# Performance work log

Hardware: AMD Instinct MI355X
Metric: run time of the kernel (lower is better)

## Reference

```python
import jax, jax.numpy as jnp
import numpy as np

LAYER_START = 4
WS = 2  # context_window_size
EPS = 1e-8


def _alpha_for_k(tf, idx):
    # tf: [L, D] per-token layer features; idx: static window row indices (last entry is k)
    Wm = tf[idx]                       # [w, D]
    w = Wm.shape[0]
    _, R = jnp.linalg.qr(Wm.T)         # reduced QR of [D, w] -> R: [w, w]
    r = R[:, -1]
    sub = R[:-1, :-1]
    coln = jnp.linalg.norm(sub, axis=0)
    align = jnp.mean(sub / coln, axis=1) @ R[:-1, -1] / jnp.linalg.norm(r[:-1])
    align = 1.0 / (align * w * 2)
    nov = jnp.abs(r[-1]) / jnp.linalg.norm(r)
    return align, nov


def _unify_token(tf):
    # tf: [L, D] -> pooled [D]
    L = tf.shape[0]
    aligns, novs = [], []
    for k in range(L):  # loop over small fixed layer count (structurally distinct windows)
        # NOTE: original torch code token_feature[k-ws:k] yields an EMPTY slice for k < ws
        left = list(range(k - WS, k)) if k >= WS else []
        right = list(range(k + 1, min(k + WS + 1, L)))
        idx = np.array(left + right + [k], dtype=np.int32)
        a, n = _alpha_for_k(tf, idx)
        aligns.append(a)
        novs.append(n)
    aa = jnp.stack(aligns)
    nv = jnp.stack(novs)
    aa = aa / aa.sum()
    nv = nv / nv.sum()
    alpha = aa + nv
    alpha = alpha / alpha.sum()
    return tf.T @ alpha


def _token_var(tf):
    # tf: [L, D] -> variance (unbiased) of subdiagonal of cosine-sim map
    w = jnp.linalg.norm(tf, axis=1, keepdims=True)
    sim = (tf @ tf.T) / jnp.clip(w * w.T, EPS)
    return jnp.var(jnp.diagonal(sim, -1), ddof=1)


def reference(all_hidden_states, attention_mask):
    # all_hidden_states: [B, num_layers, S, D]; attention_mask: [B, S] (all sentences equal length)
    T = int(np.asarray(attention_mask).sum(axis=1)[0]) - 1  # unmask_num = sum(mask) - 1
    sf = all_hidden_states[:, LAYER_START:, :T, :]          # [B, L, T, D]
    per_tok = jax.vmap(jax.vmap(_unify_token, in_axes=1))(sf)  # [B, T, D]

    def per_sentence(s, ose):
        v = jax.vmap(_token_var, in_axes=1)(s)  # [T]
        v = v / v.sum()
        return ose.T @ v                        # [D]

    return jax.vmap(per_sentence)(sf, per_tok)  # [B, D]


def setup_inputs():
    key = jax.random.key(0)
    all_hidden_states = jax.random.normal(key, (8, 12, 512, 768), dtype=jnp.float32)
    attention_mask = jnp.ones((8, 512), dtype=jnp.int32)
    return {"all_hidden_states": all_hidden_states, "attention_mask": attention_mask}
```

## Files before the change

kernel.cpp:

```cpp
#include <hip/hip_runtime.h>
#include <math.h>

#define NLAYER_TOT 12
#define LAYER0 4
#define SMAX 512
#define DIM 768

__global__ void k_init(const int* __restrict__ mask, int* __restrict__ wsT,
                       float* __restrict__ out) {
    __shared__ int red[512];
    int tid = threadIdx.x;
    red[tid] = mask[tid];
    __syncthreads();
    for (int s = 256; s >= 1; s >>= 1) {
        if (tid < s) red[tid] += red[tid + s];
        __syncthreads();
    }
    if (tid == 0) wsT[0] = red[0] - 1;
    for (int i = tid; i < 8 * DIM; i += 512) out[i] = 0.0f;
}

__global__ __launch_bounds__(64) void k_gram(const float* __restrict__ in,
                                             const int* __restrict__ wsT,
                                             float* __restrict__ Gout) {
    int T = wsT[0];
    int t = blockIdx.x;
    int b = blockIdx.y;
    if (t >= T) return;
    int lane = threadIdx.x;
    const float* base = in + ((size_t)(b * NLAYER_TOT + LAYER0) * SMAX + t) * DIM;
    float acc[36];
#pragma unroll
    for (int p = 0; p < 36; ++p) acc[p] = 0.0f;
#pragma unroll
    for (int it = 0; it < 3; ++it) {
        int d = it * 256 + lane * 4;
        float4 x[8];
#pragma unroll
        for (int k = 0; k < 8; ++k)
            x[k] = *(const float4*)(base + (size_t)k * SMAX * DIM + d);
        int p = 0;
#pragma unroll
        for (int i = 0; i < 8; ++i)
#pragma unroll
            for (int j = i; j < 8; ++j) {
                acc[p] += x[i].x * x[j].x + x[i].y * x[j].y + x[i].z * x[j].z + x[i].w * x[j].w;
                ++p;
            }
    }
    float* gdst = Gout + ((size_t)b * SMAX + t) * 36;
#pragma unroll
    for (int p = 0; p < 36; ++p) {
        float v = acc[p];
#pragma unroll
        for (int off = 32; off >= 1; off >>= 1) v += __shfl_xor(v, off, 64);
        if (lane == 0) gdst[p] = v;
    }
}

template <int W>
__device__ inline void alpha_nov(const float* __restrict__ Gf, const int* __restrict__ idx,
                                 float& align_o, float& nov_o) {
    float Gs[W][W];
#pragma unroll
    for (int i = 0; i < W; ++i)
#pragma unroll
        for (int j = i; j < W; ++j) {
            float v = Gf[idx[i] * 8 + idx[j]];
            Gs[i][j] = v;
            Gs[j][i] = v;
        }
    float R[W][W];
#pragma unroll
    for (int j = 0; j < W; ++j) {
#pragma unroll
        for (int i = 0; i <= j; ++i) {
            float s = Gs[i][j];
#pragma unroll
            for (int q = 0; q < i; ++q) s -= R[q][i] * R[q][j];
            R[i][j] = (i == j) ? sqrtf(s) : (s / R[i][i]);
        }
    }
    float ic[W - 1];
#pragma unroll
    for (int j = 0; j < W - 1; ++j) ic[j] = 1.0f / sqrtf(Gs[j][j]);
    float m[W - 1];
#pragma unroll
    for (int i = 0; i < W - 1; ++i) {
        float s = 0.0f;
#pragma unroll
        for (int j = i; j < W - 1; ++j) s += R[i][j] * ic[j];
        m[i] = s * (1.0f / (float)(W - 1));
    }
    float num = 0.0f, n1 = 0.0f;
#pragma unroll
    for (int i = 0; i < W - 1; ++i) {
        num += m[i] * R[i][W - 1];
        n1 += R[i][W - 1] * R[i][W - 1];
    }
    float align_raw = num / sqrtf(n1);
    align_o = 1.0f / (align_raw * (float)W * 2.0f);
    nov_o = fabsf(R[W - 1][W - 1]) / sqrtf(Gs[W - 1][W - 1]);
}

__global__ __launch_bounds__(64) void k_alpha(const int* __restrict__ wsT,
                                              const float* __restrict__ Gin,
                                              float* __restrict__ alpha,
                                              float* __restrict__ vraw) {
    int T = wsT[0];
    int id = blockIdx.x * 64 + threadIdx.x;
    int b = id >> 9;
    int t = id & 511;
    if (b >= 8 || t >= T) return;
    float Gf[64];
    const float* gsrc = Gin + ((size_t)b * SMAX + t) * 36;
    {
        int p = 0;
#pragma unroll
        for (int i = 0; i < 8; ++i)
#pragma unroll
            for (int j = i; j < 8; ++j) {
                float v = gsrc[p++];
                Gf[i * 8 + j] = v;
                Gf[j * 8 + i] = v;
            }
    }
    static constexpr int IDX0[5] = {1, 2, 0, 0, 0};
    static constexpr int IDX1[5] = {2, 3, 1, 0, 0};
    static constexpr int IDX2[5] = {0, 1, 3, 4, 2};
    static constexpr int IDX3[5] = {1, 2, 4, 5, 3};
    static constexpr int IDX4[5] = {2, 3, 5, 6, 4};
    static constexpr int IDX5[5] = {3, 4, 6, 7, 5};
    static constexpr int IDX6[5] = {4, 5, 7, 6, 0};
    static constexpr int IDX7[5] = {5, 6, 7, 0, 0};
    float a[8], n[8];
    alpha_nov<3>(Gf, IDX0, a[0], n[0]);
    alpha_nov<3>(Gf, IDX1, a[1], n[1]);
    alpha_nov<5>(Gf, IDX2, a[2], n[2]);
    alpha_nov<5>(Gf, IDX3, a[3], n[3]);
    alpha_nov<5>(Gf, IDX4, a[4], n[4]);
    alpha_nov<5>(Gf, IDX5, a[5], n[5]);
    alpha_nov<4>(Gf, IDX6, a[6], n[6]);
    alpha_nov<3>(Gf, IDX7, a[7], n[7]);
    float sa = 0.0f, sn = 0.0f;
#pragma unroll
    for (int k = 0; k < 8; ++k) { sa += a[k]; sn += n[k]; }
    float isa = 1.0f / sa, isn = 1.0f / sn;
    float al[8], ss = 0.0f;
#pragma unroll
    for (int k = 0; k < 8; ++k) { al[k] = a[k] * isa + n[k] * isn; ss += al[k]; }
    float iss = 1.0f / ss;
    float* adst = alpha + ((size_t)b * SMAX + t) * 8;
#pragma unroll
    for (int k = 0; k < 8; ++k) adst[k] = al[k] * iss;
    float c[7], mu = 0.0f;
#pragma unroll
    for (int i = 0; i < 7; ++i) {
        float denom = sqrtf(Gf[i * 8 + i]) * sqrtf(Gf[(i + 1) * 8 + (i + 1)]);
        denom = denom > 1e-8f ? denom : 1e-8f;
        c[i] = Gf[(i + 1) * 8 + i] / denom;
        mu += c[i];
    }
    mu *= (1.0f / 7.0f);
    float var = 0.0f;
#pragma unroll
    for (int i = 0; i < 7; ++i) var += (c[i] - mu) * (c[i] - mu);
    vraw[(size_t)b * SMAX + t] = var * (1.0f / 6.0f);
}

__global__ void k_weights(const int* __restrict__ wsT, const float* __restrict__ alpha,
                          const float* __restrict__ vraw, float* __restrict__ W) {
    int T = wsT[0];
    int b = blockIdx.x;
    int tid = threadIdx.x;
    __shared__ float red[256];
    float s = 0.0f;
    for (int t = tid; t < T; t += 256) s += vraw[(size_t)b * SMAX + t];
    red[tid] = s;
    __syncthreads();
    for (int k = 128; k >= 1; k >>= 1) {
        if (tid < k) red[tid] += red[tid + k];
        __syncthreads();
    }
    float inv = 1.0f / red[0];
    for (int t = tid; t < T; t += 256) {
        float v = vraw[(size_t)b * SMAX + t] * inv;
#pragma unroll
        for (int k = 0; k < 8; ++k)
            W[((size_t)b * SMAX + t) * 8 + k] = alpha[((size_t)b * SMAX + t) * 8 + k] * v;
    }
}

__global__ void k_out(const float* __restrict__ in, const int* __restrict__ wsT,
                      const float* __restrict__ W, float* __restrict__ out) {
    int T = wsT[0];
    int tseg = blockIdx.x;
    int dchunk = blockIdx.y;
    int b = blockIdx.z;
    int d = dchunk * 256 + threadIdx.x;
    int t0 = tseg * 16;
    int t1 = min(t0 + 16, T);
    if (t0 >= t1) return;
    const float* base = in + ((size_t)(b * NLAYER_TOT + LAYER0) * SMAX) * DIM + d;
    const float* wb = W + (size_t)b * SMAX * 8;
    float acc = 0.0f;
    for (int t = t0; t < t1; ++t) {
#pragma unroll
        for (int k = 0; k < 8; ++k)
            acc += wb[t * 8 + k] * base[((size_t)k * SMAX + t) * DIM];
    }
    atomicAdd(&out[b * DIM + d], acc);
}

extern "C" void kernel_launch(void* const* d_in, const int* in_sizes, int n_in,
                              void* d_out, int out_size, void* d_ws, size_t ws_size,
                              hipStream_t stream) {
    const float* hs = (const float*)d_in[0];
    const int* mask = (const int*)d_in[1];
    float* out = (float*)d_out;
    char* ws = (char*)d_ws;
    int* wsT = (int*)ws;
    float* G = (float*)(ws + 256);
    float* alpha = (float*)(ws + 256 + (size_t)8 * 512 * 36 * 4);
    float* vraw = (float*)(ws + 256 + (size_t)(8 * 512 * 36 + 8 * 512 * 8) * 4);
    float* W = (float*)(ws + 256 + (size_t)(8 * 512 * 36 + 8 * 512 * 8 + 8 * 512) * 4);

    k_init<<<1, 512, 0, stream>>>(mask, wsT, out);
    k_gram<<<dim3(SMAX - 1, 8), 64, 0, stream>>>(hs, wsT, G);
    k_alpha<<<64, 64, 0, stream>>>(wsT, G, alpha, vraw);
    k_weights<<<8, 256, 0, stream>>>(wsT, alpha, vraw, W);
    k_out<<<dim3(32, 3, 8), 256, 0, stream>>>(hs, wsT, W, out);
}
```

Baseline: 249.6 us.

## Fuse gram, alpha, weights and output into one kernel with deferred normalization

Merges the gram, alpha/variance, weight and output-accumulation kernels into a single per-token kernel. The gram reduction is broadcast to all lanes, every lane redundantly computes the alpha weights, and the token's own rows are re-read (likely from cache) to accumulate a weighted sum into the output with atomics. Normalization by the variance sum is deferred to a small scale kernel, using an atomically accumulated per-sentence sum. This removes the intermediate global buffers and two launches, and swaps divides and sqrts for fast rcp/rsq intrinsics, at the cost of heavy float atomics on 768 output addresses per sentence and slightly lower precision.

```diff
diff --git a/kernel.cpp b/kernel.cpp
--- a/kernel.cpp
+++ b/kernel.cpp
@@ -6,8 +6,16 @@
 #define SMAX 512
 #define DIM 768
 
+__host__ __device__ constexpr int gp(int i, int j) {
+    return (i <= j) ? (i * 8 - i * (i - 1) / 2 + (j - i))
+                    : (j * 8 - j * (j - 1) / 2 + (i - j));
+}
+
+__device__ inline float frcp(float x) { return __builtin_amdgcn_rcpf(x); }
+__device__ inline float frsq(float x) { return __builtin_amdgcn_rsqf(x); }
+
 __global__ void k_init(const int* __restrict__ mask, int* __restrict__ wsT,
-                       float* __restrict__ out) {
+                       float* __restrict__ out, float* __restrict__ vsum) {
     __shared__ int red[512];
     int tid = threadIdx.x;
     red[tid] = mask[tid];
@@ -18,17 +26,66 @@
     }
     if (tid == 0) wsT[0] = red[0] - 1;
     for (int i = tid; i < 8 * DIM; i += 512) out[i] = 0.0f;
+    if (tid < 8) vsum[tid] = 0.0f;
 }
 
-__global__ __launch_bounds__(64) void k_gram(const float* __restrict__ in,
-                                             const int* __restrict__ wsT,
-                                             float* __restrict__ Gout) {
+template <int W>
+__device__ inline void alpha_nov(const float (&A)[36], const int (&idx)[5],
+                                 float& align_o, float& nov_o) {
+    float Gs[W][W];
+#pragma unroll
+    for (int i = 0; i < W; ++i)
+#pragma unroll
+        for (int j = i; j < W; ++j) {
+            float v = A[gp(idx[i], idx[j])];
+            Gs[i][j] = v;
+            Gs[j][i] = v;
+        }
+    float R[W][W];
+#pragma unroll
+    for (int j = 0; j < W; ++j) {
+#pragma unroll
+        for (int i = 0; i <= j; ++i) {
+            float s = Gs[i][j];
+#pragma unroll
+            for (int q = 0; q < i; ++q) s -= R[q][i] * R[q][j];
+            if (i == j) R[i][j] = s * frsq(s);
+            else        R[i][j] = s * frcp(R[i][i]);
+        }
+    }
+    float ic[W - 1];
+#pragma unroll
+    for (int j = 0; j < W - 1; ++j) ic[j] = frsq(Gs[j][j]);
+    float m[W - 1];
+#pragma unroll
+    for (int i = 0; i < W - 1; ++i) {
+        float s = 0.0f;
+#pragma unroll
+        for (int j = i; j < W - 1; ++j) s += R[i][j] * ic[j];
+        m[i] = s * (1.0f / (float)(W - 1));
+    }
+    float num = 0.0f, n1 = 0.0f;
+#pragma unroll
+    for (int i = 0; i < W - 1; ++i) {
+        num += m[i] * R[i][W - 1];
+        n1 += R[i][W - 1] * R[i][W - 1];
+    }
+    float align_raw = num * frsq(n1);
+    align_o = frcp(align_raw * (float)W * 2.0f);
+    nov_o = fabsf(R[W - 1][W - 1]) * frsq(Gs[W - 1][W - 1]);
+}
+
+__global__ __launch_bounds__(64) void k_fused(const float* __restrict__ in,
+                                              const int* __restrict__ wsT,
+                                              float* __restrict__ out,
+                                              float* __restrict__ vsum) {
     int T = wsT[0];
     int t = blockIdx.x;
     int b = blockIdx.y;
     if (t >= T) return;
     int lane = threadIdx.x;
     const float* base = in + ((size_t)(b * NLAYER_TOT + LAYER0) * SMAX + t) * DIM;
+
     float acc[36];
 #pragma unroll
     for (int p = 0; p < 36; ++p) acc[p] = 0.0f;
@@ -48,83 +105,12 @@
                 ++p;
             }
     }
-    float* gdst = Gout + ((size_t)b * SMAX + t) * 36;
 #pragma unroll
     for (int p = 0; p < 36; ++p) {
-        float v = acc[p];
 #pragma unroll
-        for (int off = 32; off >= 1; off >>= 1) v += __shfl_xor(v, off, 64);
-        if (lane == 0) gdst[p] = v;
+        for (int off = 32; off >= 1; off >>= 1) acc[p] += __shfl_xor(acc[p], off, 64);
     }
-}
 
-template <int W>
-__device__ inline void alpha_nov(const float* __restrict__ Gf, const int* __restrict__ idx,
-                                 float& align_o, float& nov_o) {
-    float Gs[W][W];
-#pragma unroll
-    for (int i = 0; i < W; ++i)
-#pragma unroll
-        for (int j = i; j < W; ++j) {
-            float v = Gf[idx[i] * 8 + idx[j]];
-            Gs[i][j] = v;
-            Gs[j][i] = v;
-        }
-    float R[W][W];
-#pragma unroll
-    for (int j = 0; j < W; ++j) {
-#pragma unroll
-        for (int i = 0; i <= j; ++i) {
-            float s = Gs[i][j];
-#pragma unroll
-            for (int q = 0; q < i; ++q) s -= R[q][i] * R[q][j];
-            R[i][j] = (i == j) ? sqrtf(s) : (s / R[i][i]);
-        }
-    }
-    float ic[W - 1];
-#pragma unroll
-    for (int j = 0; j < W - 1; ++j) ic[j] = 1.0f / sqrtf(Gs[j][j]);
-    float m[W - 1];
-#pragma unroll
-    for (int i = 0; i < W - 1; ++i) {
-        float s = 0.0f;
-#pragma unroll
-        for (int j = i; j < W - 1; ++j) s += R[i][j] * ic[j];
-        m[i] = s * (1.0f / (float)(W - 1));
-    }
-    float num = 0.0f, n1 = 0.0f;
-#pragma unroll
-    for (int i = 0; i < W - 1; ++i) {
-        num += m[i] * R[i][W - 1];
-        n1 += R[i][W - 1] * R[i][W - 1];
-    }
-    float align_raw = num / sqrtf(n1);
-    align_o = 1.0f / (align_raw * (float)W * 2.0f);
-    nov_o = fabsf(R[W - 1][W - 1]) / sqrtf(Gs[W - 1][W - 1]);
-}
-
-__global__ __launch_bounds__(64) void k_alpha(const int* __restrict__ wsT,
-                                              const float* __restrict__ Gin,
-                                              float* __restrict__ alpha,
-                                              float* __restrict__ vraw) {
-    int T = wsT[0];
-    int id = blockIdx.x * 64 + threadIdx.x;
-    int b = id >> 9;
-    int t = id & 511;
-    if (b >= 8 || t >= T) return;
-    float Gf[64];
-    const float* gsrc = Gin + ((size_t)b * SMAX + t) * 36;
-    {
-        int p = 0;
-#pragma unroll
-        for (int i = 0; i < 8; ++i)
-#pragma unroll
-            for (int j = i; j < 8; ++j) {
-                float v = gsrc[p++];
-                Gf[i * 8 + j] = v;
-                Gf[j * 8 + i] = v;
-            }
-    }
     static constexpr int IDX0[5] = {1, 2, 0, 0, 0};
     static constexpr int IDX1[5] = {2, 3, 1, 0, 0};
     static constexpr int IDX2[5] = {0, 1, 3, 4, 2};
@@ -134,82 +120,64 @@
     static constexpr int IDX6[5] = {4, 5, 7, 6, 0};
     static constexpr int IDX7[5] = {5, 6, 7, 0, 0};
     float a[8], n[8];
-    alpha_nov<3>(Gf, IDX0, a[0], n[0]);
-    alpha_nov<3>(Gf, IDX1, a[1], n[1]);
-    alpha_nov<5>(Gf, IDX2, a[2], n[2]);
-    alpha_nov<5>(Gf, IDX3, a[3], n[3]);
-    alpha_nov<5>(Gf, IDX4, a[4], n[4]);
-    alpha_nov<5>(Gf, IDX5, a[5], n[5]);
-    alpha_nov<4>(Gf, IDX6, a[6], n[6]);
-    alpha_nov<3>(Gf, IDX7, a[7], n[7]);
+    alpha_nov<3>(acc, IDX0, a[0], n[0]);
+    alpha_nov<3>(acc, IDX1, a[1], n[1]);
+    alpha_nov<5>(acc, IDX2, a[2], n[2]);
+    alpha_nov<5>(acc, IDX3, a[3], n[3]);
+    alpha_nov<5>(acc, IDX4, a[4], n[4]);
+    alpha_nov<5>(acc, IDX5, a[5], n[5]);
+    alpha_nov<4>(acc, IDX6, a[6], n[6]);
+    alpha_nov<3>(acc, IDX7, a[7], n[7]);
     float sa = 0.0f, sn = 0.0f;
 #pragma unroll
     for (int k = 0; k < 8; ++k) { sa += a[k]; sn += n[k]; }
-    float isa = 1.0f / sa, isn = 1.0f / sn;
+    float isa = frcp(sa), isn = frcp(sn);
     float al[8], ss = 0.0f;
 #pragma unroll
     for (int k = 0; k < 8; ++k) { al[k] = a[k] * isa + n[k] * isn; ss += al[k]; }
-    float iss = 1.0f / ss;
-    float* adst = alpha + ((size_t)b * SMAX + t) * 8;
-#pragma unroll
-    for (int k = 0; k < 8; ++k) adst[k] = al[k] * iss;
+    float iss = frcp(ss);
+
     float c[7], mu = 0.0f;
 #pragma unroll
     for (int i = 0; i < 7; ++i) {
-        float denom = sqrtf(Gf[i * 8 + i]) * sqrtf(Gf[(i + 1) * 8 + (i + 1)]);
-        denom = denom > 1e-8f ? denom : 1e-8f;
-        c[i] = Gf[(i + 1) * 8 + i] / denom;
+        float denom = acc[gp(i, i)] * acc[gp(i + 1, i + 1)];
+        c[i] = acc[gp(i, i + 1)] * frsq(denom > 1e-16f ? denom : 1e-16f);
         mu += c[i];
     }
     mu *= (1.0f / 7.0f);
     float var = 0.0f;
 #pragma unroll
     for (int i = 0; i < 7; ++i) var += (c[i] - mu) * (c[i] - mu);
-    vraw[(size_t)b * SMAX + t] = var * (1.0f / 6.0f);
-}
+    float vraw = var * (1.0f / 6.0f);
 
-__global__ void k_weights(const int* __restrict__ wsT, const float* __restrict__ alpha,
-                          const float* __restrict__ vraw, float* __restrict__ W) {
-    int T = wsT[0];
-    int b = blockIdx.x;
-    int tid = threadIdx.x;
-    __shared__ float red[256];
-    float s = 0.0f;
-    for (int t = tid; t < T; t += 256) s += vraw[(size_t)b * SMAX + t];
-    red[tid] = s;
-    __syncthreads();
-    for (int k = 128; k >= 1; k >>= 1) {
-        if (tid < k) red[tid] += red[tid + k];
-        __syncthreads();
-    }
-    float inv = 1.0f / red[0];
-    for (int t = tid; t < T; t += 256) {
-        float v = vraw[(size_t)b * SMAX + t] * inv;
+    if (lane == 0) atomicAdd(&vsum[b], vraw);
+
+    float p8[8];
 #pragma unroll
-        for (int k = 0; k < 8; ++k)
-            W[((size_t)b * SMAX + t) * 8 + k] = alpha[((size_t)b * SMAX + t) * 8 + k] * v;
+    for (int k = 0; k < 8; ++k) p8[k] = al[k] * iss * vraw;
+    float* od = out + (size_t)b * DIM;
+#pragma unroll
+    for (int it = 0; it < 3; ++it) {
+        int d = it * 256 + lane * 4;
+        float4 s = make_float4(0.f, 0.f, 0.f, 0.f);
+#pragma unroll
+        for (int k = 0; k < 8; ++k) {
+            float4 x = *(const float4*)(base + (size_t)k * SMAX * DIM + d);
+            s.x += p8[k] * x.x; s.y += p8[k] * x.y;
+            s.z += p8[k] * x.z; s.w += p8[k] * x.w;
+        }
+        atomicAdd(&od[d + 0], s.x);
+        atomicAdd(&od[d + 1], s.y);
+        atomicAdd(&od[d + 2], s.z);
+        atomicAdd(&od[d + 3], s.w);
     }
 }
 
-__global__ void k_out(const float* __restrict__ in, const int* __restrict__ wsT,
-                      const float* __restrict__ W, float* __restrict__ out) {
-    int T = wsT[0];
-    int tseg = blockIdx.x;
-    int dchunk = blockIdx.y;
-    int b = blockIdx.z;
-    int d = dchunk * 256 + threadIdx.x;
-    int t0 = tseg * 16;
-    int t1 = min(t0 + 16, T);
-    if (t0 >= t1) return;
-    const float* base = in + ((size_t)(b * NLAYER_TOT + LAYER0) * SMAX) * DIM + d;
-    const float* wb = W + (size_t)b * SMAX * 8;
-    float acc = 0.0f;
-    for (int t = t0; t < t1; ++t) {
-#pragma unroll
-        for (int k = 0; k < 8; ++k)
-            acc += wb[t * 8 + k] * base[((size_t)k * SMAX + t) * DIM];
-    }
-    atomicAdd(&out[b * DIM + d], acc);
+__global__ void k_scale(float* __restrict__ out, const float* __restrict__ vsum) {
+    int i = blockIdx.x * blockDim.x + threadIdx.x;
+    if (i >= 8 * DIM) return;
+    int b = i / DIM;
+    out[i] = out[i] / vsum[b];
 }
 
 extern "C" void kernel_launch(void* const* d_in, const int* in_sizes, int n_in,
@@ -220,14 +188,9 @@
     float* out = (float*)d_out;
     char* ws = (char*)d_ws;
     int* wsT = (int*)ws;
-    float* G = (float*)(ws + 256);
-    float* alpha = (float*)(ws + 256 + (size_t)8 * 512 * 36 * 4);
-    float* vraw = (float*)(ws + 256 + (size_t)(8 * 512 * 36 + 8 * 512 * 8) * 4);
-    float* W = (float*)(ws + 256 + (size_t)(8 * 512 * 36 + 8 * 512 * 8 + 8 * 512) * 4);
+    float* vsum = (float*)(ws + 256);
 
-    k_init<<<1, 512, 0, stream>>>(mask, wsT, out);
-    k_gram<<<dim3(SMAX - 1, 8), 64, 0, stream>>>(hs, wsT, G);
-    k_alpha<<<64, 64, 0, stream>>>(wsT, G, alpha, vraw);
-    k_weights<<<8, 256, 0, stream>>>(wsT, alpha, vraw, W);
-    k_out<<<dim3(32, 3, 8), 256, 0, stream>>>(hs, wsT, W, out);
+    k_init<<<1, 512, 0, stream>>>(mask, wsT, out, vsum);
+    k_fused<<<dim3(SMAX - 1, 8), 64, 0, stream>>>(hs, wsT, out, vsum);
+    k_scale<<<(8 * DIM + 255) / 256, 256, 0, stream>>>(out, vsum);
 }
```

After: 311.9 us. 1.25x slower.
